# Optimization experiments

Hardware: AMD Instinct MI355X
Metric: run time of the kernel (lower is better)

The kernel has to match this reference:

```python
import jax, jax.numpy as jnp
import numpy as np

DT = 0.1
LN_EPS = 1e-5
B, T, D_IN, H, N_APP = 128, 2048, 16, 256, 10


def layer_norm(x, g, b):
    mu = jnp.mean(x, axis=-1, keepdims=True)
    var = jnp.mean(jnp.square(x - mu), axis=-1, keepdims=True)
    return (x - mu) * jax.lax.rsqrt(var + LN_EPS) * g + b


def setup_inputs() -> dict:
    key = jax.random.key(0)
    ks = jax.random.split(key, 4)
    x = jax.random.normal(ks[0], (B, T, D_IN), dtype=jnp.float32)
    W_in = jax.random.normal(ks[1], (H, D_IN), dtype=jnp.float32) * (1.0 / np.sqrt(D_IN))
    b_in = jnp.zeros((H,), dtype=jnp.float32)
    tau_param = jnp.ones((H,), dtype=jnp.float32)
    # xavier_uniform for (H, H)
    limit = np.sqrt(6.0 / (H + H))
    W_rec = jax.random.uniform(ks[2], (H, H), dtype=jnp.float32, minval=-limit, maxval=limit)
    g_intra = jnp.ones((H,), dtype=jnp.float32)
    b_intra = jnp.zeros((H,), dtype=jnp.float32)
    g_norm = jnp.ones((H,), dtype=jnp.float32)
    b_norm = jnp.zeros((H,), dtype=jnp.float32)
    W_head = jax.random.normal(ks[3], (H, N_APP), dtype=jnp.float32) * (1.0 / np.sqrt(H))
    b_head = jnp.zeros((N_APP,), dtype=jnp.float32)
    return dict(x=x, W_in=W_in, b_in=b_in, tau_param=tau_param, W_rec=W_rec,
                g_intra=g_intra, b_intra=b_intra, g_norm=g_norm, b_norm=b_norm,
                W_head=W_head, b_head=b_head)


def reference(x, W_in, b_in, tau_param, W_rec, g_intra, b_intra, g_norm, b_norm, W_head, b_head):
    # x: (B, T, D_IN)
    tau = jax.nn.softplus(tau_param)  # (H,), fixed
    # Precompute input projection for all timesteps: (B, T, H)
    inp_proj = jnp.einsum('bti,hi->bth', x, W_in) + b_in
    xs = jnp.swapaxes(inp_proj, 0, 1)  # (T, B, H) for scan

    def step(h, u_t):
        rec = h @ W_rec                       # (B, H)
        f_t = jnp.tanh(layer_norm(u_t + rec, g_intra, b_intra))
        dh = (-h / tau + f_t) * DT
        h_new = jnp.clip(h + dh, -10.0, 10.0)
        return h_new, None

    h0 = jnp.zeros((x.shape[0], W_rec.shape[0]), dtype=x.dtype)
    h, _ = jax.lax.scan(step, h0, xs)
    h = layer_norm(h, g_norm, b_norm)
    return h @ W_head + b_head  # (B, N_APP)
```

## Files before the change

### kernel.cpp

```cpp
#include <hip/hip_runtime.h>


#define BB     128
#define TT     2048
#define DIN    16
#define HH     256
#define NAPP   10
#define NT     256
#define DT_STEP 0.1f
#define LN_EPS_C 1e-5f
#define LOG2E2  2.8853900817779268f

typedef _Float16 half2_t __attribute__((ext_vector_type(2)));

template<int CTRL>
__device__ __forceinline__ float dpp_mov0(float x) {
    return __builtin_bit_cast(float,
        __builtin_amdgcn_update_dpp(0, __builtin_bit_cast(int, x), CTRL, 0xF, 0xF, true));
}

__device__ __forceinline__ void wave_reduce2(float& s1, float& s2) {
    s1 += dpp_mov0<0x111>(s1); s2 += dpp_mov0<0x111>(s2);
    s1 += dpp_mov0<0x112>(s1); s2 += dpp_mov0<0x112>(s2);
    s1 += dpp_mov0<0x114>(s1); s2 += dpp_mov0<0x114>(s2);
    s1 += dpp_mov0<0x118>(s1); s2 += dpp_mov0<0x118>(s2);
    s1 += dpp_mov0<0x142>(s1); s2 += dpp_mov0<0x142>(s2);
    s1 += dpp_mov0<0x143>(s1); s2 += dpp_mov0<0x143>(s2);
}

__device__ __forceinline__ half2_t as_h2(int v) { return __builtin_bit_cast(half2_t, v); }
__device__ __forceinline__ float rl63(float v) {
    return __builtin_bit_cast(float,
        __builtin_amdgcn_readlane(__builtin_bit_cast(int, v), 63));
}
__device__ __forceinline__ float softplus_f(float v) {
    return (v > 20.f) ? v : log1pf(__expf(v));
}
__device__ __forceinline__ float exp2_fast(float v) {
    float r;
    asm("v_exp_f32 %0, %1" : "=v"(r) : "v"(v));
    return r;
}

__global__ __launch_bounds__(NT, 1)
void liquid_scan_kernel(const float* __restrict__ x,
                        const float* __restrict__ W_in,
                        const float* __restrict__ b_in,
                        const float* __restrict__ tau_param,
                        const float* __restrict__ W_rec,
                        const float* __restrict__ g_intra,
                        const float* __restrict__ b_intra,
                        const float* __restrict__ g_norm,
                        const float* __restrict__ b_norm,
                        const float* __restrict__ W_head,
                        const float* __restrict__ b_head,
                        float* __restrict__ out)
{
    const int tid  = threadIdx.x;
    const int b    = blockIdx.x;
    const int lane = tid & 63;
    const int kq   = tid >> 6;
    const int j0   = lane * 4;

    __shared__ __align__(16) float    x_lds[TT * DIN];
    __shared__ __align__(16) float    part[2][4][HH];
    __shared__ __align__(16) unsigned flags[4];

    {
        const float4* xg = (const float4*)(x + (size_t)b * TT * DIN);
        float4* xl = (float4*)x_lds;
        #pragma unroll 4
        for (int i = tid; i < TT * DIN / 4; i += NT) xl[i] = xg[i];
    }
    if (tid < 4) flags[tid] = 0u;

    half2_t w2[4][32];
    #pragma unroll
    for (int p = 0; p < 32; ++p) {
        const float* r0 = W_rec + (size_t)(64 * kq + 2 * p) * HH + j0;
        const float* r1 = r0 + HH;
        #pragma unroll
        for (int c = 0; c < 4; ++c) {
            half2_t t2; t2.x = (_Float16)r0[c]; t2.y = (_Float16)r1[c];
            w2[c][p] = t2;
        }
    }

    float win[4][4];
    #pragma unroll
    for (int c = 0; c < 4; ++c) {
        #pragma unroll
        for (int r = 0; r < 4; ++r)
            win[c][r] = W_in[(size_t)(j0 + c) * DIN + 4 * kq + r];
    }

    float bi_[4], gi2_[4], bbi2_[4], dec_[4], gn_[4], bn_[4];
    {
        const float4 v0 = *(const float4*)(b_in      + j0);
        const float4 v1 = *(const float4*)(g_intra   + j0);
        const float4 v2 = *(const float4*)(b_intra   + j0);
        const float4 v3 = *(const float4*)(tau_param + j0);
        const float4 v4 = *(const float4*)(g_norm    + j0);
        const float4 v5 = *(const float4*)(b_norm    + j0);
        bi_[0] = v0.x; bi_[1] = v0.y; bi_[2] = v0.z; bi_[3] = v0.w;
        gi2_[0] = v1.x * LOG2E2; gi2_[1] = v1.y * LOG2E2;
        gi2_[2] = v1.z * LOG2E2; gi2_[3] = v1.w * LOG2E2;
        bbi2_[0] = v2.x * LOG2E2; bbi2_[1] = v2.y * LOG2E2;
        bbi2_[2] = v2.z * LOG2E2; bbi2_[3] = v2.w * LOG2E2;
        dec_[0] = 1.f - DT_STEP / softplus_f(v3.x);
        dec_[1] = 1.f - DT_STEP / softplus_f(v3.y);
        dec_[2] = 1.f - DT_STEP / softplus_f(v3.z);
        dec_[3] = 1.f - DT_STEP / softplus_f(v3.w);
        gn_[0] = v4.x; gn_[1] = v4.y; gn_[2] = v4.z; gn_[3] = v4.w;
        bn_[0] = v5.x; bn_[1] = v5.y; bn_[2] = v5.z; bn_[3] = v5.w;
    }

    float hj[4] = {0.f, 0.f, 0.f, 0.f};
    int pkX = 0, pkY = 0;
    const int rlbase = 16 * kq;
    const int o1 = (kq + 1) & 3, o2 = (kq + 2) & 3, o3 = (kq + 3) & 3;
    volatile unsigned* vfl = (volatile unsigned*)flags;

    __syncthreads();

    #pragma unroll 1
    for (int t = 0; t < TT; ++t) {
        const float4 xs = *(const float4*)&x_lds[t * DIN + 4 * kq];

        float a0 = 0.f, a1 = 0.f, a2 = 0.f, a3 = 0.f;
        #pragma unroll
        for (int p = 0; p < 32; ++p) {
            const int r = __builtin_amdgcn_readlane((p & 1) ? pkY : pkX,
                                                    rlbase + (p >> 1));
            a0 = __builtin_amdgcn_fdot2(as_h2(r), w2[0][p], a0, false);
            a1 = __builtin_amdgcn_fdot2(as_h2(r), w2[1][p], a1, false);
            a2 = __builtin_amdgcn_fdot2(as_h2(r), w2[2][p], a2, false);
            a3 = __builtin_amdgcn_fdot2(as_h2(r), w2[3][p], a3, false);
        }
        a0 = fmaf(xs.x, win[0][0], a0); a0 = fmaf(xs.y, win[0][1], a0);
        a0 = fmaf(xs.z, win[0][2], a0); a0 = fmaf(xs.w, win[0][3], a0);
        a1 = fmaf(xs.x, win[1][0], a1); a1 = fmaf(xs.y, win[1][1], a1);
        a1 = fmaf(xs.z, win[1][2], a1); a1 = fmaf(xs.w, win[1][3], a1);
        a2 = fmaf(xs.x, win[2][0], a2); a2 = fmaf(xs.y, win[2][1], a2);
        a2 = fmaf(xs.z, win[2][2], a2); a2 = fmaf(xs.w, win[2][3], a2);
        a3 = fmaf(xs.x, win[3][0], a3); a3 = fmaf(xs.y, win[3][1], a3);
        a3 = fmaf(xs.z, win[3][2], a3); a3 = fmaf(xs.w, win[3][3], a3);

        const unsigned tgt = (unsigned)(t + 1);
        ((float4*)part[t & 1][kq])[lane] = make_float4(a0, a1, a2, a3);
        asm volatile("s_waitcnt lgkmcnt(0)" ::: "memory");
        if (lane == 0) vfl[kq] = tgt;
        unsigned f1, f2, f3;
        do {
            f1 = vfl[o1]; f2 = vfl[o2]; f3 = vfl[o3];
        } while (f1 < tgt || f2 < tgt || f3 < tgt);
        asm volatile("" ::: "memory");

        const float4 p1 = ((const float4*)part[t & 1][o1])[lane];
        const float4 p2 = ((const float4*)part[t & 1][o2])[lane];
        const float4 p3 = ((const float4*)part[t & 1][o3])[lane];
        float u[4];
        u[0] = (a0 + p1.x) + (p2.x + p3.x) + bi_[0];
        u[1] = (a1 + p1.y) + (p2.y + p3.y) + bi_[1];
        u[2] = (a2 + p1.z) + (p2.z + p3.z) + bi_[2];
        u[3] = (a3 + p1.w) + (p2.w + p3.w) + bi_[3];

        float s1 = (u[0] + u[1]) + (u[2] + u[3]);
        float s2 = (u[0] * u[0] + u[1] * u[1]) + (u[2] * u[2] + u[3] * u[3]);
        wave_reduce2(s1, s2);
        const float S1 = rl63(s1);
        const float S2 = rl63(s2);
        const float mu  = S1 * (1.f / HH);
        const float var = S2 * (1.f / HH) - mu * mu;
        const float rs  = __builtin_amdgcn_rsqf(var + LN_EPS_C);
        #pragma unroll
        for (int c = 0; c < 4; ++c) {
            const float xn2 = fmaf((u[c] - mu) * rs, gi2_[c], bbi2_[c]);
            const float e   = exp2_fast(xn2);
            const float r   = __builtin_amdgcn_rcpf(e + 1.f);
            const float fdt = fmaf(-2.f * DT_STEP, r, DT_STEP);
            float v = fmaf(hj[c], dec_[c], fdt);
            v = fminf(10.f, fmaxf(-10.f, v));
            hj[c] = v;
        }
        pkX = __builtin_bit_cast(int, __builtin_amdgcn_cvt_pkrtz(hj[0], hj[1]));
        pkY = __builtin_bit_cast(int, __builtin_amdgcn_cvt_pkrtz(hj[2], hj[3]));
    }

    if (kq == 0) {
        float s1 = (hj[0] + hj[1]) + (hj[2] + hj[3]);
        float s2 = (hj[0] * hj[0] + hj[1] * hj[1]) + (hj[2] * hj[2] + hj[3] * hj[3]);
        wave_reduce2(s1, s2);
        const float S1 = rl63(s1);
        const float S2 = rl63(s2);
        const float mu  = S1 * (1.f / HH);
        const float var = S2 * (1.f / HH) - mu * mu;
        const float rs  = rsqrtf(var + LN_EPS_C);
        float4 ho;
        ho.x = (hj[0] - mu) * rs * gn_[0] + bn_[0];
        ho.y = (hj[1] - mu) * rs * gn_[1] + bn_[1];
        ho.z = (hj[2] - mu) * rs * gn_[2] + bn_[2];
        ho.w = (hj[3] - mu) * rs * gn_[3] + bn_[3];
        ((float4*)part[0][0])[lane] = ho;
    }
    __syncthreads();
    if (tid < NAPP) {
        float o = b_head[tid];
        for (int jj = 0; jj < HH; ++jj)
            o = fmaf(part[0][0][jj], W_head[jj * NAPP + tid], o);
        out[(size_t)b * NAPP + tid] = o;
    }
}

extern "C" void kernel_launch(void* const* d_in, const int* in_sizes, int n_in,
                              void* d_out, int out_size, void* d_ws, size_t ws_size,
                              hipStream_t stream) {
    const float* x       = (const float*)d_in[0];
    const float* W_in    = (const float*)d_in[1];
    const float* b_in    = (const float*)d_in[2];
    const float* tau     = (const float*)d_in[3];
    const float* W_rec   = (const float*)d_in[4];
    const float* g_intra = (const float*)d_in[5];
    const float* b_intra = (const float*)d_in[6];
    const float* g_norm  = (const float*)d_in[7];
    const float* b_norm  = (const float*)d_in[8];
    const float* W_head  = (const float*)d_in[9];
    const float* b_head  = (const float*)d_in[10];
    float* out = (float*)d_out;

    hipLaunchKernelGGL(liquid_scan_kernel, dim3(BB), dim3(NT), 0, stream,
                       x, W_in, b_in, tau, W_rec, g_intra, b_intra,
                       g_norm, b_norm, W_head, b_head, out);
}
```

Measured before the change: 1.906 ms.

## Replace LDS flag spin-wait with barrier and split dot-product accumulator chains

The per-step cross-wave handoff now uses __syncthreads instead of volatile LDS flags polled in a spin loop. The fdot2 reduction is split into four independent accumulator chains per output, shortening the serial dependency chain. The clamp becomes a single med3. A full barrier has a fixed cost per step, and the split chains need more registers, which could pressure occupancy or cause spills next to the large w2 register array.

```diff
diff --git a/kernel.cpp b/kernel.cpp
--- a/kernel.cpp
+++ b/kernel.cpp
@@ -62,9 +62,8 @@
     const int kq   = tid >> 6;
     const int j0   = lane * 4;
 
-    __shared__ __align__(16) float    x_lds[TT * DIN];
-    __shared__ __align__(16) float    part[2][4][HH];
-    __shared__ __align__(16) unsigned flags[4];
+    __shared__ __align__(16) float x_lds[TT * DIN];
+    __shared__ __align__(16) float part[2][4][HH];
 
     {
         const float4* xg = (const float4*)(x + (size_t)b * TT * DIN);
@@ -72,7 +71,6 @@
         #pragma unroll 4
         for (int i = tid; i < TT * DIN / 4; i += NT) xl[i] = xg[i];
     }
-    if (tid < 4) flags[tid] = 0u;
 
     half2_t w2[4][32];
     #pragma unroll
@@ -119,7 +117,6 @@
     int pkX = 0, pkY = 0;
     const int rlbase = 16 * kq;
     const int o1 = (kq + 1) & 3, o2 = (kq + 2) & 3, o3 = (kq + 3) & 3;
-    volatile unsigned* vfl = (volatile unsigned*)flags;
 
     __syncthreads();
 
@@ -127,43 +124,54 @@
     for (int t = 0; t < TT; ++t) {
         const float4 xs = *(const float4*)&x_lds[t * DIN + 4 * kq];
 
-        float a0 = 0.f, a1 = 0.f, a2 = 0.f, a3 = 0.f;
-        #pragma unroll
-        for (int p = 0; p < 32; ++p) {
-            const int r = __builtin_amdgcn_readlane((p & 1) ? pkY : pkX,
-                                                    rlbase + (p >> 1));
-            a0 = __builtin_amdgcn_fdot2(as_h2(r), w2[0][p], a0, false);
-            a1 = __builtin_amdgcn_fdot2(as_h2(r), w2[1][p], a1, false);
-            a2 = __builtin_amdgcn_fdot2(as_h2(r), w2[2][p], a2, false);
-            a3 = __builtin_amdgcn_fdot2(as_h2(r), w2[3][p], a3, false);
-        }
-        a0 = fmaf(xs.x, win[0][0], a0); a0 = fmaf(xs.y, win[0][1], a0);
-        a0 = fmaf(xs.z, win[0][2], a0); a0 = fmaf(xs.w, win[0][3], a0);
-        a1 = fmaf(xs.x, win[1][0], a1); a1 = fmaf(xs.y, win[1][1], a1);
-        a1 = fmaf(xs.z, win[1][2], a1); a1 = fmaf(xs.w, win[1][3], a1);
-        a2 = fmaf(xs.x, win[2][0], a2); a2 = fmaf(xs.y, win[2][1], a2);
-        a2 = fmaf(xs.z, win[2][2], a2); a2 = fmaf(xs.w, win[2][3], a2);
-        a3 = fmaf(xs.x, win[3][0], a3); a3 = fmaf(xs.y, win[3][1], a3);
-        a3 = fmaf(xs.z, win[3][2], a3); a3 = fmaf(xs.w, win[3][3], a3);
-
-        const unsigned tgt = (unsigned)(t + 1);
-        ((float4*)part[t & 1][kq])[lane] = make_float4(a0, a1, a2, a3);
-        asm volatile("s_waitcnt lgkmcnt(0)" ::: "memory");
-        if (lane == 0) vfl[kq] = tgt;
-        unsigned f1, f2, f3;
-        do {
-            f1 = vfl[o1]; f2 = vfl[o2]; f3 = vfl[o3];
-        } while (f1 < tgt || f2 < tgt || f3 < tgt);
-        asm volatile("" ::: "memory");
+        float acc[4][4];
+        #pragma unroll
+        for (int c = 0; c < 4; ++c) {
+            #pragma unroll
+            for (int i = 0; i < 4; ++i) acc[c][i] = 0.f;
+        }
+        #pragma unroll
+        for (int g = 0; g < 8; ++g) {
+            const int r0 = __builtin_amdgcn_readlane(pkX, rlbase + 2 * g);
+            const int r1 = __builtin_amdgcn_readlane(pkY, rlbase + 2 * g);
+            const int r2 = __builtin_amdgcn_readlane(pkX, rlbase + 2 * g + 1);
+            const int r3 = __builtin_amdgcn_readlane(pkY, rlbase + 2 * g + 1);
+            #pragma unroll
+            for (int c = 0; c < 4; ++c)
+                acc[c][0] = __builtin_amdgcn_fdot2(as_h2(r0), w2[c][4 * g + 0], acc[c][0], false);
+            #pragma unroll
+            for (int c = 0; c < 4; ++c)
+                acc[c][1] = __builtin_amdgcn_fdot2(as_h2(r1), w2[c][4 * g + 1], acc[c][1], false);
+            #pragma unroll
+            for (int c = 0; c < 4; ++c)
+                acc[c][2] = __builtin_amdgcn_fdot2(as_h2(r2), w2[c][4 * g + 2], acc[c][2], false);
+            #pragma unroll
+            for (int c = 0; c < 4; ++c)
+                acc[c][3] = __builtin_amdgcn_fdot2(as_h2(r3), w2[c][4 * g + 3], acc[c][3], false);
+        }
+        const float xsv[4] = {xs.x, xs.y, xs.z, xs.w};
+        #pragma unroll
+        for (int c = 0; c < 4; ++c) {
+            #pragma unroll
+            for (int i = 0; i < 4; ++i)
+                acc[c][i] = fmaf(xsv[i], win[c][i], acc[c][i]);
+        }
+        float a[4];
+        #pragma unroll
+        for (int c = 0; c < 4; ++c)
+            a[c] = (acc[c][0] + acc[c][1]) + (acc[c][2] + acc[c][3]);
+
+        ((float4*)part[t & 1][kq])[lane] = make_float4(a[0], a[1], a[2], a[3]);
+        __syncthreads();
 
         const float4 p1 = ((const float4*)part[t & 1][o1])[lane];
         const float4 p2 = ((const float4*)part[t & 1][o2])[lane];
         const float4 p3 = ((const float4*)part[t & 1][o3])[lane];
         float u[4];
-        u[0] = (a0 + p1.x) + (p2.x + p3.x) + bi_[0];
-        u[1] = (a1 + p1.y) + (p2.y + p3.y) + bi_[1];
-        u[2] = (a2 + p1.z) + (p2.z + p3.z) + bi_[2];
-        u[3] = (a3 + p1.w) + (p2.w + p3.w) + bi_[3];
+        u[0] = (a[0] + p1.x) + (p2.x + p3.x) + bi_[0];
+        u[1] = (a[1] + p1.y) + (p2.y + p3.y) + bi_[1];
+        u[2] = (a[2] + p1.z) + (p2.z + p3.z) + bi_[2];
+        u[3] = (a[3] + p1.w) + (p2.w + p3.w) + bi_[3];
 
         float s1 = (u[0] + u[1]) + (u[2] + u[3]);
         float s2 = (u[0] * u[0] + u[1] * u[1]) + (u[2] * u[2] + u[3] * u[3]);
@@ -179,9 +187,8 @@
             const float e   = exp2_fast(xn2);
             const float r   = __builtin_amdgcn_rcpf(e + 1.f);
             const float fdt = fmaf(-2.f * DT_STEP, r, DT_STEP);
-            float v = fmaf(hj[c], dec_[c], fdt);
-            v = fminf(10.f, fmaxf(-10.f, v));
-            hj[c] = v;
+            const float v   = fmaf(hj[c], dec_[c], fdt);
+            hj[c] = __builtin_amdgcn_fmed3f(v, -10.f, 10.f);
         }
         pkX = __builtin_bit_cast(int, __builtin_amdgcn_cvt_pkrtz(hj[0], hj[1]));
         pkY = __builtin_bit_cast(int, __builtin_amdgcn_cvt_pkrtz(hj[2], hj[3]));
```

New measurement: 1.576 ms. 1.21x faster.
